# Optimization experiments

Hardware: AMD Instinct MI355X
Metric: run time of the kernel (lower is better)

Reference implementation:

```python
import jax, jax.numpy as jnp
import numpy as np

N = 50000
E = 600000
IN_C = 128
HID = 128
OUT_C = 2


def setup_inputs() -> dict:
    key = jax.random.key(0)
    ks = jax.random.split(key, 16)
    x = jax.random.normal(ks[0], (N, IN_C), dtype=jnp.float32)
    edge_index = jax.random.randint(ks[1], (2, E), 0, N, dtype=jnp.int64)
    s = 0.05
    # policy_net: Linear(2*in, 64) -> ReLU -> Linear(64, 1) -> Sigmoid
    W_p1 = jax.random.normal(ks[2], (64, 2 * IN_C), dtype=jnp.float32) * s
    b_p1 = jnp.zeros((64,), dtype=jnp.float32)
    W_p2 = jax.random.normal(ks[3], (1, 64), dtype=jnp.float32) * s
    b_p2 = jnp.zeros((1,), dtype=jnp.float32)
    # GCNConv weights (lin without bias + separate bias, PyG convention)
    W1 = jax.random.normal(ks[4], (HID, IN_C), dtype=jnp.float32) * s
    b1 = jnp.zeros((HID,), dtype=jnp.float32)
    W2 = jax.random.normal(ks[5], (HID, HID), dtype=jnp.float32) * s
    b2 = jnp.zeros((HID,), dtype=jnp.float32)
    W_lin = jax.random.normal(ks[6], (OUT_C, HID), dtype=jnp.float32) * s
    b_lin = jnp.zeros((OUT_C,), dtype=jnp.float32)
    return {"x": x, "edge_index": edge_index, "W_p1": W_p1, "b_p1": b_p1,
            "W_p2": W_p2, "b_p2": b_p2, "W1": W1, "b1": b1, "W2": W2,
            "b2": b2, "W_lin": W_lin, "b_lin": b_lin}


def gcn_conv(x, src, dst, edge_weight, W, b, n_nodes):
    # PyG GCNConv with normalize=True, add_self_loops=True, given edge_weight.
    loop = jnp.arange(n_nodes, dtype=src.dtype)
    s = jnp.concatenate([src, loop])
    d = jnp.concatenate([dst, loop])
    w = jnp.concatenate([edge_weight, jnp.ones((n_nodes,), x.dtype)])
    deg = jax.ops.segment_sum(w, d, num_segments=n_nodes)
    dinv = jnp.where(deg > 0, jax.lax.rsqrt(jnp.where(deg > 0, deg, 1.0)), 0.0)
    norm = dinv[s] * w * dinv[d]  # [E+N]
    xl = x @ W.T  # [N, out]
    msg = norm[:, None] * xl[s]  # gather + scale
    agg = jax.ops.segment_sum(msg, d, num_segments=n_nodes)
    return agg + b


def reference(x, edge_index, W_p1, b_p1, W_p2, b_p2, W1, b1, W2, b2, W_lin, b_lin):
    src, dst = edge_index[0], edge_index[1]
    # edge-weight policy MLP on gathered, concatenated endpoint features
    cat_feat = jnp.concatenate([x[src], x[dst]], axis=1)  # [E, 2*in]
    h = jax.nn.relu(cat_feat @ W_p1.T + b_p1)
    edge_weight = jax.nn.sigmoid(h @ W_p2.T + b_p2)[:, 0]  # [E]
    x1 = jax.nn.relu(gcn_conv(x, src, dst, edge_weight, W1, b1, N))
    x2 = jax.nn.relu(gcn_conv(x1, src, dst, edge_weight, W2, b2, N))
    out = x2 @ W_lin.T + b_lin
    return jax.nn.sigmoid(out)
```

## Files before the change

### kernel.cpp

```cpp
#include <hip/hip_runtime.h>
#include <hip/hip_bf16.h>

#define NN 50000
#define NE 600000
#define CPAD 16

typedef __attribute__((ext_vector_type(8))) short short8;
typedef __attribute__((ext_vector_type(8))) _Float16 half8;
typedef __attribute__((ext_vector_type(4))) float floatx4;

__device__ __forceinline__ short bf16_bits(float v) {
    __hip_bfloat16 h = __float2bfloat16(v);
    return *reinterpret_cast<short*>(&h);
}

__device__ __forceinline__ void stage_w(const short* __restrict__ src, short* lds) {
    int t = threadIdx.x;
#pragma unroll
    for (int i = 0; i < 8; ++i) {
        int gci = t + i * 256;
        int row = gci >> 4, ci = gci & 15;
        short8 v = *(const short8*)(src + gci * 8);
        *(short8*)(lds + row * 128 + ((ci ^ (row & 7)) << 3)) = v;
    }
}

__global__ void k_init_cvt(const int* __restrict__ raw, int* __restrict__ count,
                           int* __restrict__ flag, const float* __restrict__ wp1,
                           const float* __restrict__ w1, const float* __restrict__ w2,
                           __hip_bfloat16* __restrict__ wcatb, __hip_bfloat16* __restrict__ w1b,
                           __hip_bfloat16* __restrict__ w2b) {
    int i = blockIdx.x * blockDim.x + threadIdx.x;
    if (i < NN) {
        count[(size_t)i * CPAD] = 0;
    }
    if (i < 16384) {
        int r = i >> 7, c = i & 127;
        float v = (r < 64) ? wp1[r * 256 + c] : wp1[(r - 64) * 256 + 128 + c];
        wcatb[i] = __float2bfloat16(v);
    } else if (i < 32768) {
        w1b[i - 16384] = __float2bfloat16(w1[i - 16384]);
    } else if (i < 49152) {
        w2b[i - 32768] = __float2bfloat16(w2[i - 32768]);
    }
    if (blockIdx.x == 0) {
        if (threadIdx.x == 0) *flag = 0;
        __syncthreads();
        int any = 0;
        for (int j = threadIdx.x; j < 1024; j += 256) any |= raw[2 * j + 1];
        if (any) atomicOr(flag, 1);
    }
}

#define GG 782
__global__ __launch_bounds__(256) void k_uv(
    const float* __restrict__ x, const __hip_bfloat16* __restrict__ Wb,
    const float* __restrict__ bp1, _Float16* __restrict__ uvh,
    __hip_bfloat16* __restrict__ xb) {
    __shared__ short wlds[16384];
    stage_w((const short*)Wb, wlds);
    __syncthreads();

    const int lane = threadIdx.x & 63;
    const int wave = threadIdx.x >> 6;
    const int col = lane & 15;
    const int quad = lane >> 4;

    int tile = blockIdx.x * 4 + wave;
    if (tile >= NN / 16) return;
    int base = tile * 16;

    short8 bfrag[4][8];
    const int rx = col & 7;
#pragma unroll
    for (int tt = 0; tt < 8; ++tt) {
        int row = tt * 16 + col;
#pragma unroll
        for (int kk = 0; kk < 4; ++kk)
            bfrag[kk][tt] = *(const short8*)(wlds + row * 128 + (((kk * 4 + quad) ^ rx) << 3));
    }

    floatx4 acc[8];
#pragma unroll
    for (int t = 0; t < 8; ++t) acc[t] = (floatx4){0.f, 0.f, 0.f, 0.f};
#pragma unroll
    for (int kk = 0; kk < 4; ++kk) {
        const float* xrow = x + (size_t)(base + col) * 128 + kk * 32 + quad * 8;
        float4 f0 = ((const float4*)xrow)[0];
        float4 f1 = ((const float4*)xrow)[1];
        short8 afrag;
        afrag[0] = bf16_bits(f0.x); afrag[1] = bf16_bits(f0.y);
        afrag[2] = bf16_bits(f0.z); afrag[3] = bf16_bits(f0.w);
        afrag[4] = bf16_bits(f1.x); afrag[5] = bf16_bits(f1.y);
        afrag[6] = bf16_bits(f1.z); afrag[7] = bf16_bits(f1.w);
        *(short8*)((short*)xb + (size_t)(base + col) * 128 + kk * 32 + quad * 8) = afrag;
#pragma unroll
        for (int tt = 0; tt < 8; ++tt)
            acc[tt] = __builtin_amdgcn_mfma_f32_16x16x32_bf16(afrag, bfrag[kk][tt], acc[tt], 0, 0, 0);
    }
#pragma unroll
    for (int tt = 0; tt < 8; ++tt) {
        int n = tt * 16 + col;
        float badd = (tt >= 4) ? bp1[n - 64] : 0.f;
#pragma unroll
        for (int r = 0; r < 4; ++r) {
            int row = base + quad * 4 + r;
            uvh[(size_t)row * 128 + n] = (_Float16)(acc[tt][r] + badd);
        }
    }
}

#define GCNT 293
#define GPOL 9375
__global__ __launch_bounds__(256) void k_cnt_policy(
    const int* __restrict__ raw, const int* __restrict__ flag,
    int* __restrict__ count, int* __restrict__ rank,
    const _Float16* __restrict__ uvh, const float* __restrict__ wp2,
    const float* __restrict__ bp2, float* __restrict__ ew_flat) {
    const bool f32 = (*flag) != 0;
    const long long* r64 = (const long long*)raw;
    if (blockIdx.x < GCNT) {
        int gid = blockIdx.x * 256 + threadIdx.x;
        int e0 = gid * 8;
        if (e0 + 8 <= NE) {
            int dd[8];
            if (f32) {
#pragma unroll
                for (int k = 0; k < 8; ++k) dd[k] = raw[NE + e0 + k];
            } else {
#pragma unroll
                for (int k = 0; k < 8; ++k) dd[k] = (int)r64[NE + e0 + k];
            }
            int rk[8];
#pragma unroll
            for (int k = 0; k < 8; ++k) rk[k] = atomicAdd(&count[(size_t)dd[k] * CPAD], 1);
#pragma unroll
            for (int k = 0; k < 8; ++k) rank[e0 + k] = rk[k];
        } else {
            for (int e = e0; e < NE; ++e) {
                int d = f32 ? raw[NE + e] : (int)r64[NE + e];
                rank[e] = atomicAdd(&count[(size_t)d * CPAD], 1);
            }
        }
        return;
    }
    int pb = blockIdx.x - GCNT;
    int wave = threadIdx.x >> 6, lane = threadIdx.x & 63;
    int g = lane >> 3, c = lane & 7;
    int e1 = pb * 64 + wave * 16 + g;
    int e2 = e1 + 8;
    int s1, d1, s2, d2;
    if (f32) {
        s1 = raw[e1]; d1 = raw[NE + e1];
        s2 = raw[e2]; d2 = raw[NE + e2];
    } else {
        s1 = (int)r64[e1]; d1 = (int)r64[NE + e1];
        s2 = (int)r64[e2]; d2 = (int)r64[NE + e2];
    }
    half8 u1 = *(const half8*)(uvh + (size_t)s1 * 128 + c * 8);
    half8 v1 = *(const half8*)(uvh + (size_t)d1 * 128 + 64 + c * 8);
    half8 u2 = *(const half8*)(uvh + (size_t)s2 * 128 + c * 8);
    half8 v2 = *(const half8*)(uvh + (size_t)d2 * 128 + 64 + c * 8);
    float w2v[8];
    const float4* w2p = (const float4*)(wp2 + c * 8);
    float4 wa = w2p[0], wb = w2p[1];
    w2v[0] = wa.x; w2v[1] = wa.y; w2v[2] = wa.z; w2v[3] = wa.w;
    w2v[4] = wb.x; w2v[5] = wb.y; w2v[6] = wb.z; w2v[7] = wb.w;
    float b2 = bp2[0];
    float p1 = 0.f, p2 = 0.f;
#pragma unroll
    for (int j = 0; j < 8; ++j) {
        float h1 = (float)u1[j] + (float)v1[j];
        float h2 = (float)u2[j] + (float)v2[j];
        h1 = h1 > 0.f ? h1 : 0.f;
        h2 = h2 > 0.f ? h2 : 0.f;
        p1 += h1 * w2v[j];
        p2 += h2 * w2v[j];
    }
    p1 += __shfl_xor(p1, 1, 64); p2 += __shfl_xor(p2, 1, 64);
    p1 += __shfl_xor(p1, 2, 64); p2 += __shfl_xor(p2, 2, 64);
    p1 += __shfl_xor(p1, 4, 64); p2 += __shfl_xor(p2, 4, 64);
    if (c == 0) {
        ew_flat[e1] = 1.f / (1.f + __expf(-(p1 + b2)));
        ew_flat[e2] = 1.f / (1.f + __expf(-(p2 + b2)));
    }
}

__global__ void k_scan_block(const int* __restrict__ count, int* __restrict__ tmp,
                             int* __restrict__ bsums) {
    __shared__ int s[512];
    int tid = threadIdx.x;
    int i = blockIdx.x * 512 + tid;
    s[tid] = (i < NN) ? count[(size_t)i * CPAD] : 0;
    __syncthreads();
    for (int off = 1; off < 512; off <<= 1) {
        int t = (tid >= off) ? s[tid - off] : 0;
        __syncthreads();
        s[tid] += t;
        __syncthreads();
    }
    if (i < NN) tmp[i] = s[tid];
    if (tid == 511) bsums[blockIdx.x] = s[511];
}

__global__ void k_finalize(const int* __restrict__ tmp, const int* __restrict__ bsums,
                           int* __restrict__ rowptr) {
    __shared__ int sb[128];
    int tid = threadIdx.x;
    if (tid < 128) sb[tid] = (tid < 98) ? bsums[tid] : 0;
    __syncthreads();
    for (int off = 1; off < 128; off <<= 1) {
        int t = (tid < 128 && tid >= off) ? sb[tid - off] : 0;
        __syncthreads();
        if (tid < 128) sb[tid] += t;
        __syncthreads();
    }
    int i = blockIdx.x * blockDim.x + tid;
    if (i >= NN) return;
    int blk = i >> 9;
    int add = blk ? sb[blk - 1] : 0;
    int incl = tmp[i] + add;
    rowptr[i + 1] = incl;
    if (i == 0) rowptr[0] = 0;
}

__global__ void k_fill(const int* __restrict__ raw, const int* __restrict__ flag,
                       const int* __restrict__ rank, const int* __restrict__ rowptr,
                       const float* __restrict__ ew_flat, int2* __restrict__ meta) {
    int e = blockIdx.x * blockDim.x + threadIdx.x;
    if (e >= NE) return;
    int s, d;
    if (*flag) {
        s = raw[e];
        d = raw[NE + e];
    } else {
        const long long* r64 = (const long long*)raw;
        s = (int)r64[e];
        d = (int)r64[NE + e];
    }
    int pos = rowptr[d] + rank[e];
    meta[pos] = make_int2(s, __float_as_int(ew_flat[e]));
}

__global__ __launch_bounds__(256) void k_deg(const int* __restrict__ rowptr,
                                             const int2* __restrict__ meta,
                                             float* __restrict__ deg) {
    int wid = (blockIdx.x * blockDim.x + threadIdx.x) >> 6;
    int lane = threadIdx.x & 63;
    if (wid >= NN) return;
    int beg = rowptr[wid], end = rowptr[wid + 1];
    float s = 0.f;
    for (int p = beg + lane; p < end; p += 64) s += __int_as_float(meta[p].y);
#pragma unroll
    for (int off = 1; off < 64; off <<= 1) s += __shfl_xor(s, off, 64);
    if (lane == 0) deg[wid] = 1.f + s;
}

__global__ __launch_bounds__(256) void k_gemm(
    const __hip_bfloat16* __restrict__ A, const __hip_bfloat16* __restrict__ Wb,
    const float* __restrict__ deg, _Float16* __restrict__ xlh) {
    __shared__ short wlds[16384];
    stage_w((const short*)Wb, wlds);
    __syncthreads();

    const int lane = threadIdx.x & 63;
    const int wave = threadIdx.x >> 6;
    const int col = lane & 15;
    const int quad = lane >> 4;

    int tile = blockIdx.x * 4 + wave;
    if (tile >= NN / 16) return;
    int base = tile * 16;

    short8 bfrag[4][8];
    const int rx = col & 7;
#pragma unroll
    for (int tt = 0; tt < 8; ++tt) {
        int row = tt * 16 + col;
#pragma unroll
        for (int kk = 0; kk < 4; ++kk)
            bfrag[kk][tt] = *(const short8*)(wlds + row * 128 + (((kk * 4 + quad) ^ rx) << 3));
    }
    const short* xs = (const short*)A;

    floatx4 acc[8];
#pragma unroll
    for (int t = 0; t < 8; ++t) acc[t] = (floatx4){0.f, 0.f, 0.f, 0.f};
#pragma unroll
    for (int kk = 0; kk < 4; ++kk) {
        short8 afrag = *(const short8*)(xs + (size_t)(base + col) * 128 + kk * 32 + quad * 8);
#pragma unroll
        for (int tt = 0; tt < 8; ++tt)
            acc[tt] = __builtin_amdgcn_mfma_f32_16x16x32_bf16(afrag, bfrag[kk][tt], acc[tt], 0, 0, 0);
    }
    float di[4];
#pragma unroll
    for (int r = 0; r < 4; ++r) di[r] = rsqrtf(deg[base + quad * 4 + r]);
#pragma unroll
    for (int tt = 0; tt < 8; ++tt) {
        int n = tt * 16 + col;
#pragma unroll
        for (int r = 0; r < 4; ++r) {
            int row = base + quad * 4 + r;
            xlh[(size_t)row * 128 + n] = (_Float16)(di[r] * acc[tt][r]);
        }
    }
}

__device__ __forceinline__ void scatter_core(
    const int* __restrict__ rowptr, const int2* __restrict__ meta,
    const _Float16* __restrict__ xlh, int wid, int g, int c, float acc[8]) {
    int beg = rowptr[wid], end = rowptr[wid + 1];
    int p = beg + g;
    for (; p + 12 < end; p += 16) {
        int2 m1 = meta[p], m2 = meta[p + 4], m3 = meta[p + 8], m4 = meta[p + 12];
        half8 r1 = *(const half8*)(xlh + (size_t)m1.x * 128 + c * 8);
        half8 r2 = *(const half8*)(xlh + (size_t)m2.x * 128 + c * 8);
        half8 r3 = *(const half8*)(xlh + (size_t)m3.x * 128 + c * 8);
        half8 r4 = *(const half8*)(xlh + (size_t)m4.x * 128 + c * 8);
        float c1 = __int_as_float(m1.y), c2 = __int_as_float(m2.y);
        float c3 = __int_as_float(m3.y), c4 = __int_as_float(m4.y);
#pragma unroll
        for (int j = 0; j < 8; ++j)
            acc[j] += c1 * (float)r1[j] + c2 * (float)r2[j] + c3 * (float)r3[j] + c4 * (float)r4[j];
    }
    for (; p + 4 < end; p += 8) {
        int2 m1 = meta[p], m2 = meta[p + 4];
        half8 r1 = *(const half8*)(xlh + (size_t)m1.x * 128 + c * 8);
        half8 r2 = *(const half8*)(xlh + (size_t)m2.x * 128 + c * 8);
        float c1 = __int_as_float(m1.y), c2 = __int_as_float(m2.y);
#pragma unroll
        for (int j = 0; j < 8; ++j) acc[j] += c1 * (float)r1[j] + c2 * (float)r2[j];
    }
    if (p < end) {
        int2 m1 = meta[p];
        half8 r1 = *(const half8*)(xlh + (size_t)m1.x * 128 + c * 8);
        float c1 = __int_as_float(m1.y);
#pragma unroll
        for (int j = 0; j < 8; ++j) acc[j] += c1 * (float)r1[j];
    }
#pragma unroll
    for (int j = 0; j < 8; ++j) {
        acc[j] += __shfl_xor(acc[j], 16, 64);
        acc[j] += __shfl_xor(acc[j], 32, 64);
    }
}

__global__ __launch_bounds__(256) void k_scatter_mid(
    const int* __restrict__ rowptr, const int2* __restrict__ meta,
    const float* __restrict__ deg, const _Float16* __restrict__ xlh,
    const float* __restrict__ bias, __hip_bfloat16* __restrict__ xb2) {
    int wid = (blockIdx.x * blockDim.x + threadIdx.x) >> 6;
    int lane = threadIdx.x & 63;
    if (wid >= NN) return;
    int g = lane >> 4, c = lane & 15;
    float acc[8] = {0.f, 0.f, 0.f, 0.f, 0.f, 0.f, 0.f, 0.f};
    scatter_core(rowptr, meta, xlh, wid, g, c, acc);
    if (g == 0) {
        float dn = rsqrtf(deg[wid]);
        half8 sv = *(const half8*)(xlh + (size_t)wid * 128 + c * 8);
        const float4* bp = (const float4*)(bias + c * 8);
        float4 ba = bp[0], bb = bp[1];
        float bv[8] = {ba.x, ba.y, ba.z, ba.w, bb.x, bb.y, bb.z, bb.w};
        short8 o;
#pragma unroll
        for (int j = 0; j < 8; ++j) {
            float t = bv[j] + dn * ((float)sv[j] + acc[j]);
            t = t > 0.f ? t : 0.f;
            o[j] = bf16_bits(t);
        }
        *(short8*)((short*)xb2 + (size_t)wid * 128 + c * 8) = o;
    }
}

__global__ __launch_bounds__(256) void k_scatter_out(
    const int* __restrict__ rowptr, const int2* __restrict__ meta,
    const float* __restrict__ deg, const _Float16* __restrict__ xlh,
    const float* __restrict__ bias, const float* __restrict__ wlin,
    const float* __restrict__ blin, float* __restrict__ out) {
    int wid = (blockIdx.x * blockDim.x + threadIdx.x) >> 6;
    int lane = threadIdx.x & 63;
    if (wid >= NN) return;
    int g = lane >> 4, c = lane & 15;
    float acc[8] = {0.f, 0.f, 0.f, 0.f, 0.f, 0.f, 0.f, 0.f};
    scatter_core(rowptr, meta, xlh, wid, g, c, acc);
    if (g == 0) {
        float dn = rsqrtf(deg[wid]);
        half8 sv = *(const half8*)(xlh + (size_t)wid * 128 + c * 8);
        const float4* bp = (const float4*)(bias + c * 8);
        float4 ba = bp[0], bb = bp[1];
        float bv[8] = {ba.x, ba.y, ba.z, ba.w, bb.x, bb.y, bb.z, bb.w};
        float p0 = 0.f, p1 = 0.f;
#pragma unroll
        for (int j = 0; j < 8; ++j) {
            float t = bv[j] + dn * ((float)sv[j] + acc[j]);
            t = t > 0.f ? t : 0.f;
            p0 += t * wlin[c * 8 + j];
            p1 += t * wlin[128 + c * 8 + j];
        }
#pragma unroll
        for (int off = 1; off < 16; off <<= 1) {
            p0 += __shfl_xor(p0, off, 64);
            p1 += __shfl_xor(p1, off, 64);
        }
        if (c == 0) {
            out[wid * 2 + 0] = 1.f / (1.f + __expf(-(p0 + blin[0])));
            out[wid * 2 + 1] = 1.f / (1.f + __expf(-(p1 + blin[1])));
        }
    }
}


extern "C" void kernel_launch(void* const* d_in, const int* in_sizes, int n_in,
                              void* d_out, int out_size, void* d_ws, size_t ws_size,
                              hipStream_t stream) {
    const float* x = (const float*)d_in[0];
    const int* eidx_raw = (const int*)d_in[1];
    const float* W_p1 = (const float*)d_in[2];
    const float* b_p1 = (const float*)d_in[3];
    const float* W_p2 = (const float*)d_in[4];
    const float* b_p2 = (const float*)d_in[5];
    const float* W1 = (const float*)d_in[6];
    const float* b1 = (const float*)d_in[7];
    const float* W2 = (const float*)d_in[8];
    const float* b2 = (const float*)d_in[9];
    const float* W_lin = (const float*)d_in[10];
    const float* b_lin = (const float*)d_in[11];
    float* out = (float*)d_out;

    char* ws = (char*)d_ws;
    size_t off = 0;
    auto alloc = [&](size_t bytes) -> void* {
        off = (off + 255) & ~(size_t)255;
        void* p = ws + off;
        off += bytes;
        return p;
    };
    float* deg = (float*)alloc(NN * 4);
    int* rowptr = (int*)alloc((NN + 1) * 4);
    int* count = (int*)alloc((size_t)NN * CPAD * 4);
    int* flag = (int*)alloc(4);
    int* bsums = (int*)alloc(128 * 4);
    int* rank = (int*)alloc((size_t)NE * 4);
    float* ew_flat = (float*)alloc((size_t)NE * 4);
    int2* meta = (int2*)alloc((size_t)NE * 8);
    __hip_bfloat16* xb = (__hip_bfloat16*)alloc((size_t)NN * 128 * 2);
    _Float16* xlh = (_Float16*)alloc((size_t)NN * 128 * 2);
    _Float16* uvh = (_Float16*)alloc((size_t)NN * 128 * 2);
    __hip_bfloat16* wcatb = (__hip_bfloat16*)alloc(128 * 128 * 2);
    __hip_bfloat16* w1b = (__hip_bfloat16*)alloc(128 * 128 * 2);
    __hip_bfloat16* w2b = (__hip_bfloat16*)alloc(128 * 128 * 2);
    int* tmp = (int*)meta;

    const int TB = 256;
    int gN = (NN + TB - 1) / TB;
    int gE = (NE + TB - 1) / TB;
    int gS = (NN + 3) / 4;

    k_init_cvt<<<gN, TB, 0, stream>>>(eidx_raw, count, flag, W_p1, W1, W2, wcatb, w1b, w2b);
    k_uv<<<GG, TB, 0, stream>>>(x, wcatb, b_p1, uvh, xb);
    k_cnt_policy<<<GCNT + GPOL, TB, 0, stream>>>(eidx_raw, flag, count, rank, uvh, W_p2, b_p2, ew_flat);

    k_scan_block<<<98, 512, 0, stream>>>(count, tmp, bsums);
    k_finalize<<<gN, TB, 0, stream>>>(tmp, bsums, rowptr);
    k_fill<<<gE, TB, 0, stream>>>(eidx_raw, flag, rank, rowptr, ew_flat, meta);
    k_deg<<<gS, TB, 0, stream>>>(rowptr, meta, deg);

    k_gemm<<<GG, TB, 0, stream>>>(xb, w1b, deg, xlh);
    k_scatter_mid<<<gS, TB, 0, stream>>>(rowptr, meta, deg, xlh, b1, xb);
    k_gemm<<<GG, TB, 0, stream>>>(xb, w2b, deg, xlh);
    k_scatter_out<<<gS, TB, 0, stream>>>(rowptr, meta, deg, xlh, b2, W_lin, b_lin, out);
}
```

Baseline: 244.0 us.

## Regroup launches: fuse count with uv GEMM, finalize with policy, degree into GEMM

Edge-count atomics now run as extra blocks inside the uv GEMM launch, and the rowptr finalize runs as extra blocks alongside the policy MLP. The standalone degree kernel is gone: the first GEMM sums edge weights per row from the CSR itself. The fill kernel now handles four edges per thread. This removes launches and lets independent work share a launch, at the cost of mixing heterogeneous blocks and adding an irregular per-row loop inside the GEMM epilogue.

```diff
diff --git a/kernel.cpp b/kernel.cpp
--- a/kernel.cpp
+++ b/kernel.cpp
@@ -52,11 +52,40 @@
     }
 }
 
+#define GCNT 293
 #define GG 782
-__global__ __launch_bounds__(256) void k_uv(
+__global__ __launch_bounds__(256) void k_uv_cnt(
     const float* __restrict__ x, const __hip_bfloat16* __restrict__ Wb,
     const float* __restrict__ bp1, _Float16* __restrict__ uvh,
-    __hip_bfloat16* __restrict__ xb) {
+    __hip_bfloat16* __restrict__ xb, const int* __restrict__ raw,
+    const int* __restrict__ flag, int* __restrict__ count, int* __restrict__ rank) {
+    if (blockIdx.x < GCNT) {
+        const bool f32 = (*flag) != 0;
+        const long long* r64 = (const long long*)raw;
+        int gid = blockIdx.x * 256 + threadIdx.x;
+        int e0 = gid * 8;
+        if (e0 + 8 <= NE) {
+            int dd[8];
+            if (f32) {
+#pragma unroll
+                for (int k = 0; k < 8; ++k) dd[k] = raw[NE + e0 + k];
+            } else {
+#pragma unroll
+                for (int k = 0; k < 8; ++k) dd[k] = (int)r64[NE + e0 + k];
+            }
+            int rk[8];
+#pragma unroll
+            for (int k = 0; k < 8; ++k) rk[k] = atomicAdd(&count[(size_t)dd[k] * CPAD], 1);
+#pragma unroll
+            for (int k = 0; k < 8; ++k) rank[e0 + k] = rk[k];
+        } else {
+            for (int e = e0; e < NE; ++e) {
+                int d = f32 ? raw[NE + e] : (int)r64[NE + e];
+                rank[e] = atomicAdd(&count[(size_t)d * CPAD], 1);
+            }
+        }
+        return;
+    }
     __shared__ short wlds[16384];
     stage_w((const short*)Wb, wlds);
     __syncthreads();
@@ -66,7 +95,7 @@
     const int col = lane & 15;
     const int quad = lane >> 4;
 
-    int tile = blockIdx.x * 4 + wave;
+    int tile = (blockIdx.x - GCNT) * 4 + wave;
     if (tile >= NN / 16) return;
     int base = tile * 16;
 
@@ -107,82 +136,6 @@
             int row = base + quad * 4 + r;
             uvh[(size_t)row * 128 + n] = (_Float16)(acc[tt][r] + badd);
         }
-    }
-}
-
-#define GCNT 293
-#define GPOL 9375
-__global__ __launch_bounds__(256) void k_cnt_policy(
-    const int* __restrict__ raw, const int* __restrict__ flag,
-    int* __restrict__ count, int* __restrict__ rank,
-    const _Float16* __restrict__ uvh, const float* __restrict__ wp2,
-    const float* __restrict__ bp2, float* __restrict__ ew_flat) {
-    const bool f32 = (*flag) != 0;
-    const long long* r64 = (const long long*)raw;
-    if (blockIdx.x < GCNT) {
-        int gid = blockIdx.x * 256 + threadIdx.x;
-        int e0 = gid * 8;
-        if (e0 + 8 <= NE) {
-            int dd[8];
-            if (f32) {
-#pragma unroll
-                for (int k = 0; k < 8; ++k) dd[k] = raw[NE + e0 + k];
-            } else {
-#pragma unroll
-                for (int k = 0; k < 8; ++k) dd[k] = (int)r64[NE + e0 + k];
-            }
-            int rk[8];
-#pragma unroll
-            for (int k = 0; k < 8; ++k) rk[k] = atomicAdd(&count[(size_t)dd[k] * CPAD], 1);
-#pragma unroll
-            for (int k = 0; k < 8; ++k) rank[e0 + k] = rk[k];
-        } else {
-            for (int e = e0; e < NE; ++e) {
-                int d = f32 ? raw[NE + e] : (int)r64[NE + e];
-                rank[e] = atomicAdd(&count[(size_t)d * CPAD], 1);
-            }
-        }
-        return;
-    }
-    int pb = blockIdx.x - GCNT;
-    int wave = threadIdx.x >> 6, lane = threadIdx.x & 63;
-    int g = lane >> 3, c = lane & 7;
-    int e1 = pb * 64 + wave * 16 + g;
-    int e2 = e1 + 8;
-    int s1, d1, s2, d2;
-    if (f32) {
-        s1 = raw[e1]; d1 = raw[NE + e1];
-        s2 = raw[e2]; d2 = raw[NE + e2];
-    } else {
-        s1 = (int)r64[e1]; d1 = (int)r64[NE + e1];
-        s2 = (int)r64[e2]; d2 = (int)r64[NE + e2];
-    }
-    half8 u1 = *(const half8*)(uvh + (size_t)s1 * 128 + c * 8);
-    half8 v1 = *(const half8*)(uvh + (size_t)d1 * 128 + 64 + c * 8);
-    half8 u2 = *(const half8*)(uvh + (size_t)s2 * 128 + c * 8);
-    half8 v2 = *(const half8*)(uvh + (size_t)d2 * 128 + 64 + c * 8);
-    float w2v[8];
-    const float4* w2p = (const float4*)(wp2 + c * 8);
-    float4 wa = w2p[0], wb = w2p[1];
-    w2v[0] = wa.x; w2v[1] = wa.y; w2v[2] = wa.z; w2v[3] = wa.w;
-    w2v[4] = wb.x; w2v[5] = wb.y; w2v[6] = wb.z; w2v[7] = wb.w;
-    float b2 = bp2[0];
-    float p1 = 0.f, p2 = 0.f;
-#pragma unroll
-    for (int j = 0; j < 8; ++j) {
-        float h1 = (float)u1[j] + (float)v1[j];
-        float h2 = (float)u2[j] + (float)v2[j];
-        h1 = h1 > 0.f ? h1 : 0.f;
-        h2 = h2 > 0.f ? h2 : 0.f;
-        p1 += h1 * w2v[j];
-        p2 += h2 * w2v[j];
-    }
-    p1 += __shfl_xor(p1, 1, 64); p2 += __shfl_xor(p2, 1, 64);
-    p1 += __shfl_xor(p1, 2, 64); p2 += __shfl_xor(p2, 2, 64);
-    p1 += __shfl_xor(p1, 4, 64); p2 += __shfl_xor(p2, 4, 64);
-    if (c == 0) {
-        ew_flat[e1] = 1.f / (1.f + __expf(-(p1 + b2)));
-        ew_flat[e2] = 1.f / (1.f + __expf(-(p2 + b2)));
     }
 }
 
@@ -203,62 +156,106 @@
     if (tid == 511) bsums[blockIdx.x] = s[511];
 }
 
-__global__ void k_finalize(const int* __restrict__ tmp, const int* __restrict__ bsums,
-                           int* __restrict__ rowptr) {
-    __shared__ int sb[128];
-    int tid = threadIdx.x;
-    if (tid < 128) sb[tid] = (tid < 98) ? bsums[tid] : 0;
-    __syncthreads();
-    for (int off = 1; off < 128; off <<= 1) {
-        int t = (tid < 128 && tid >= off) ? sb[tid - off] : 0;
+#define GFIN 196
+#define GPOL 9375
+__global__ __launch_bounds__(256) void k_fin_policy(
+    const int* __restrict__ tmp, const int* __restrict__ bsums, int* __restrict__ rowptr,
+    const int* __restrict__ raw, const int* __restrict__ flag,
+    const _Float16* __restrict__ uvh, const float* __restrict__ wp2,
+    const float* __restrict__ bp2, float* __restrict__ ew_flat) {
+    if (blockIdx.x < GFIN) {
+        __shared__ int sb[128];
+        int tid = threadIdx.x;
+        if (tid < 128) sb[tid] = (tid < 98) ? bsums[tid] : 0;
         __syncthreads();
-        if (tid < 128) sb[tid] += t;
-        __syncthreads();
-    }
-    int i = blockIdx.x * blockDim.x + tid;
-    if (i >= NN) return;
-    int blk = i >> 9;
-    int add = blk ? sb[blk - 1] : 0;
-    int incl = tmp[i] + add;
-    rowptr[i + 1] = incl;
-    if (i == 0) rowptr[0] = 0;
+        for (int off = 1; off < 128; off <<= 1) {
+            int t = (tid < 128 && tid >= off) ? sb[tid - off] : 0;
+            __syncthreads();
+            if (tid < 128) sb[tid] += t;
+            __syncthreads();
+        }
+        int i = blockIdx.x * 256 + tid;
+        if (i >= NN) return;
+        int blk = i >> 9;
+        int add = blk ? sb[blk - 1] : 0;
+        rowptr[i + 1] = tmp[i] + add;
+        if (i == 0) rowptr[0] = 0;
+        return;
+    }
+    const bool f32 = (*flag) != 0;
+    const long long* r64 = (const long long*)raw;
+    int pb = blockIdx.x - GFIN;
+    int wave = threadIdx.x >> 6, lane = threadIdx.x & 63;
+    int g = lane >> 3, c = lane & 7;
+    int e1 = pb * 64 + wave * 16 + g;
+    int e2 = e1 + 8;
+    int s1, d1, s2, d2;
+    if (f32) {
+        s1 = raw[e1]; d1 = raw[NE + e1];
+        s2 = raw[e2]; d2 = raw[NE + e2];
+    } else {
+        s1 = (int)r64[e1]; d1 = (int)r64[NE + e1];
+        s2 = (int)r64[e2]; d2 = (int)r64[NE + e2];
+    }
+    half8 u1 = *(const half8*)(uvh + (size_t)s1 * 128 + c * 8);
+    half8 v1 = *(const half8*)(uvh + (size_t)d1 * 128 + 64 + c * 8);
+    half8 u2 = *(const half8*)(uvh + (size_t)s2 * 128 + c * 8);
+    half8 v2 = *(const half8*)(uvh + (size_t)d2 * 128 + 64 + c * 8);
+    float w2v[8];
+    const float4* w2p = (const float4*)(wp2 + c * 8);
+    float4 wa = w2p[0], wb = w2p[1];
+    w2v[0] = wa.x; w2v[1] = wa.y; w2v[2] = wa.z; w2v[3] = wa.w;
+    w2v[4] = wb.x; w2v[5] = wb.y; w2v[6] = wb.z; w2v[7] = wb.w;
+    float b2 = bp2[0];
+    float p1 = 0.f, p2 = 0.f;
+#pragma unroll
+    for (int j = 0; j < 8; ++j) {
+        float h1 = (float)u1[j] + (float)v1[j];
+        float h2 = (float)u2[j] + (float)v2[j];
+        h1 = h1 > 0.f ? h1 : 0.f;
+        h2 = h2 > 0.f ? h2 : 0.f;
+        p1 += h1 * w2v[j];
+        p2 += h2 * w2v[j];
+    }
+    p1 += __shfl_xor(p1, 1, 64); p2 += __shfl_xor(p2, 1, 64);
+    p1 += __shfl_xor(p1, 2, 64); p2 += __shfl_xor(p2, 2, 64);
+    p1 += __shfl_xor(p1, 4, 64); p2 += __shfl_xor(p2, 4, 64);
+    if (c == 0) {
+        ew_flat[e1] = 1.f / (1.f + __expf(-(p1 + b2)));
+        ew_flat[e2] = 1.f / (1.f + __expf(-(p2 + b2)));
+    }
 }
 
 __global__ void k_fill(const int* __restrict__ raw, const int* __restrict__ flag,
                        const int* __restrict__ rank, const int* __restrict__ rowptr,
                        const float* __restrict__ ew_flat, int2* __restrict__ meta) {
-    int e = blockIdx.x * blockDim.x + threadIdx.x;
-    if (e >= NE) return;
-    int s, d;
-    if (*flag) {
-        s = raw[e];
-        d = raw[NE + e];
-    } else {
-        const long long* r64 = (const long long*)raw;
-        s = (int)r64[e];
-        d = (int)r64[NE + e];
-    }
-    int pos = rowptr[d] + rank[e];
-    meta[pos] = make_int2(s, __float_as_int(ew_flat[e]));
-}
-
-__global__ __launch_bounds__(256) void k_deg(const int* __restrict__ rowptr,
-                                             const int2* __restrict__ meta,
-                                             float* __restrict__ deg) {
-    int wid = (blockIdx.x * blockDim.x + threadIdx.x) >> 6;
-    int lane = threadIdx.x & 63;
-    if (wid >= NN) return;
-    int beg = rowptr[wid], end = rowptr[wid + 1];
-    float s = 0.f;
-    for (int p = beg + lane; p < end; p += 64) s += __int_as_float(meta[p].y);
-#pragma unroll
-    for (int off = 1; off < 64; off <<= 1) s += __shfl_xor(s, off, 64);
-    if (lane == 0) deg[wid] = 1.f + s;
-}
-
+    int t = blockIdx.x * blockDim.x + threadIdx.x;
+    int e0 = t * 4;
+    if (e0 >= NE) return;
+    const bool f32 = (*flag) != 0;
+    const long long* r64 = (const long long*)raw;
+    int s[4], d[4], rk[4];
+    float ew[4];
+#pragma unroll
+    for (int k = 0; k < 4; ++k) {
+        int e = e0 + k;
+        if (f32) { s[k] = raw[e]; d[k] = raw[NE + e]; }
+        else     { s[k] = (int)r64[e]; d[k] = (int)r64[NE + e]; }
+        rk[k] = rank[e];
+        ew[k] = ew_flat[e];
+    }
+    int base[4];
+#pragma unroll
+    for (int k = 0; k < 4; ++k) base[k] = rowptr[d[k]];
+#pragma unroll
+    for (int k = 0; k < 4; ++k) meta[base[k] + rk[k]] = make_int2(s[k], __float_as_int(ew[k]));
+}
+
+template <bool CDEG>
 __global__ __launch_bounds__(256) void k_gemm(
     const __hip_bfloat16* __restrict__ A, const __hip_bfloat16* __restrict__ Wb,
-    const float* __restrict__ deg, _Float16* __restrict__ xlh) {
+    const int* __restrict__ rowptr, const int2* __restrict__ meta,
+    float* __restrict__ deg, _Float16* __restrict__ xlh) {
     __shared__ short wlds[16384];
     stage_w((const short*)Wb, wlds);
     __syncthreads();
@@ -294,8 +291,21 @@
             acc[tt] = __builtin_amdgcn_mfma_f32_16x16x32_bf16(afrag, bfrag[kk][tt], acc[tt], 0, 0, 0);
     }
     float di[4];
-#pragma unroll
-    for (int r = 0; r < 4; ++r) di[r] = rsqrtf(deg[base + quad * 4 + r]);
+    if (CDEG) {
+        int rn = base + col;
+        int beg = rowptr[rn], end = rowptr[rn + 1];
+        float sdeg = 0.f;
+        for (int p = beg + quad; p < end; p += 4) sdeg += __int_as_float(meta[p].y);
+        sdeg += __shfl_xor(sdeg, 16, 64);
+        sdeg += __shfl_xor(sdeg, 32, 64);
+        float dv = 1.f + sdeg;
+        if (quad == 0) deg[rn] = dv;
+#pragma unroll
+        for (int r = 0; r < 4; ++r) di[r] = rsqrtf(__shfl(dv, quad * 4 + r, 64));
+    } else {
+#pragma unroll
+        for (int r = 0; r < 4; ++r) di[r] = rsqrtf(deg[base + quad * 4 + r]);
+    }
 #pragma unroll
     for (int tt = 0; tt < 8; ++tt) {
         int n = tt * 16 + col;
@@ -454,20 +464,17 @@
 
     const int TB = 256;
     int gN = (NN + TB - 1) / TB;
-    int gE = (NE + TB - 1) / TB;
+    int gF = (NE / 4 + TB - 1) / TB;
     int gS = (NN + 3) / 4;
 
     k_init_cvt<<<gN, TB, 0, stream>>>(eidx_raw, count, flag, W_p1, W1, W2, wcatb, w1b, w2b);
-    k_uv<<<GG, TB, 0, stream>>>(x, wcatb, b_p1, uvh, xb);
-    k_cnt_policy<<<GCNT + GPOL, TB, 0, stream>>>(eidx_raw, flag, count, rank, uvh, W_p2, b_p2, ew_flat);
-
+    k_uv_cnt<<<GCNT + GG, TB, 0, stream>>>(x, wcatb, b_p1, uvh, xb, eidx_raw, flag, count, rank);
     k_scan_block<<<98, 512, 0, stream>>>(count, tmp, bsums);
-    k_finalize<<<gN, TB, 0, stream>>>(tmp, bsums, rowptr);
-    k_fill<<<gE, TB, 0, stream>>>(eidx_raw, flag, rank, rowptr, ew_flat, meta);
-    k_deg<<<gS, TB, 0, stream>>>(rowptr, meta, deg);
-
-    k_gemm<<<GG, TB, 0, stream>>>(xb, w1b, deg, xlh);
+    k_fin_policy<<<GFIN + GPOL, TB, 0, stream>>>(tmp, bsums, rowptr, eidx_raw, flag, uvh,
+                                                 W_p2, b_p2, ew_flat);
+    k_fill<<<gF, TB, 0, stream>>>(eidx_raw, flag, rank, rowptr, ew_flat, meta);
+    k_gemm<true><<<GG, TB, 0, stream>>>(xb, w1b, rowptr, meta, deg, xlh);
     k_scatter_mid<<<gS, TB, 0, stream>>>(rowptr, meta, deg, xlh, b1, xb);
-    k_gemm<<<GG, TB, 0, stream>>>(xb, w2b, deg, xlh);
+    k_gemm<false><<<GG, TB, 0, stream>>>(xb, w2b, rowptr, meta, deg, xlh);
     k_scatter_out<<<gS, TB, 0, stream>>>(rowptr, meta, deg, xlh, b2, W_lin, b_lin, out);
 }
```

Measured after the change: 237.2 us. 1.03x faster.
